# Performance work log

Hardware: AMD Instinct MI355X
Metric: run time of the kernel (lower is better)

Reference implementation:

```python
import jax, jax.numpy as jnp
import numpy as np

H, KVH, HD = 16, 8, 64
EPS = 1e-6
SCALING = HD ** -0.5


def _rms_norm(x, w):
    # RMSNorm over last dim (head_dim)
    var = jnp.mean(x * x, axis=-1, keepdims=True)
    return x * jax.lax.rsqrt(var + EPS) * w


def _rotate_half(x):
    x1, x2 = jnp.split(x, 2, axis=-1)
    return jnp.concatenate([-x2, x1], axis=-1)


def setup_inputs() -> dict:
    key = jax.random.key(0)
    ks = jax.random.split(key, 12)
    B, Q, CTX, HID = 1, 2048, 2048, 1024
    NB, T = 32, 64  # Q == NB * T
    TOTAL = CTX + Q
    inp = {}
    inp["hidden_states"] = jax.random.normal(ks[0], (B, Q, HID), jnp.float32)
    inp["target_hidden"] = jax.random.normal(ks[1], (B, CTX, HID), jnp.float32)
    pos = jnp.arange(TOTAL, dtype=jnp.float32)[:, None]
    inv = 1.0 / (10000.0 ** (jnp.arange(0, HD, 2, dtype=jnp.float32) / HD))
    ang = pos * inv[None, :]
    emb = jnp.concatenate([ang, ang], axis=-1)
    inp["cos"] = jnp.cos(emb)[None]  # [B, TOTAL, HD]
    inp["sin"] = jnp.sin(emb)[None]
    inp["attention_mask"] = jnp.zeros((B, 1, Q, TOTAL), jnp.float32)
    s = 0.02
    inp["Wq"] = jax.random.normal(ks[2], (HID, H * HD), jnp.float32) * s
    inp["Wk"] = jax.random.normal(ks[3], (HID, KVH * HD), jnp.float32) * s
    inp["Wv"] = jax.random.normal(ks[4], (HID, KVH * HD), jnp.float32) * s
    inp["Wo"] = jax.random.normal(ks[5], (H * HD, HID), jnp.float32) * s
    inp["q_norm_w"] = jnp.ones((HD,), jnp.float32)
    inp["k_norm_w"] = jnp.ones((HD,), jnp.float32)
    inp["tree_bias"] = jax.random.normal(ks[6], (64, H), jnp.float32) * s
    inp["relation_map"] = jax.random.randint(ks[7], (B, NB, T, T), 0, 64, jnp.int32)
    return inp


def reference(hidden_states, target_hidden, cos, sin, attention_mask,
              Wq, Wk, Wv, Wo, q_norm_w, k_norm_w, tree_bias, relation_map):
    B, Q, HID = hidden_states.shape
    CTX = target_hidden.shape[1]
    TOTAL = CTX + Q
    NB, T = relation_map.shape[1], relation_map.shape[2]
    groups = H // KVH

    q = (hidden_states @ Wq).reshape(B, Q, H, HD)
    k_ctx = target_hidden @ Wk
    k_noise = hidden_states @ Wk
    v_ctx = target_hidden @ Wv
    v_noise = hidden_states @ Wv
    k = jnp.concatenate([k_ctx, k_noise], axis=1).reshape(B, TOTAL, KVH, HD)
    v = jnp.concatenate([v_ctx, v_noise], axis=1).reshape(B, TOTAL, KVH, HD)

    q = _rms_norm(q, q_norm_w).transpose(0, 2, 1, 3)  # [B,H,Q,HD]
    k = _rms_norm(k, k_norm_w).transpose(0, 2, 1, 3)  # [B,KVH,TOTAL,HD]
    v = v.transpose(0, 2, 1, 3)

    cos_b = cos[:, None]  # [B,1,TOTAL,HD]
    sin_b = sin[:, None]
    q = q * cos_b[..., -Q:, :] + _rotate_half(q) * sin_b[..., -Q:, :]
    k = k * cos_b + _rotate_half(k) * sin_b

    # GQA: repeat kv heads
    k = jnp.repeat(k, groups, axis=1)  # [B,H,TOTAL,HD]
    v = jnp.repeat(v, groups, axis=1)

    scores = jnp.einsum('bhqd,bhkd->bhqk', q, k) * SCALING  # [B,H,Q,TOTAL]
    scores = scores + attention_mask

    # tree positional bias: block-diagonal (same tree) on the noise-noise block
    bias = tree_bias[relation_map]                 # [B,NB,T,T,H]
    bias = jnp.transpose(bias, (0, 4, 1, 2, 3))    # [B,H,NB,T,T]
    s_noise = scores[..., CTX:].reshape(B, H, NB, T, NB, T)
    idx = jnp.arange(NB)
    s_noise = s_noise.at[:, :, idx, :, idx, :].add(jnp.transpose(bias, (2, 0, 1, 3, 4)))
    scores = jnp.concatenate([scores[..., :CTX], s_noise.reshape(B, H, Q, Q)], axis=-1)

    attn = jax.nn.softmax(scores, axis=-1)
    out = jnp.einsum('bhqk,bhkd->bhqd', attn, v)   # [B,H,Q,HD]
    out = out.transpose(0, 2, 1, 3).reshape(B, Q, H * HD)
    return out @ Wo
```

## Files before the change

kernel.cpp:

```cpp
#include <hip/hip_runtime.h>
#include <hip/hip_bf16.h>

typedef __bf16 bf16x8 __attribute__((ext_vector_type(8)));
typedef float  f32x4  __attribute__((ext_vector_type(4)));

__device__ inline unsigned short f2bf(float f) {
    unsigned int u = __float_as_uint(f);
    u += 0x7fffu + ((u >> 16) & 1u);
    return (unsigned short)(u >> 16);
}
__device__ inline float bf2f(unsigned int s) {
    return __uint_as_float(s << 16);
}
__device__ inline unsigned int pk2bf(float a, float b) {
    __hip_bfloat162 h = __float22bfloat162_rn(make_float2(a, b));
    union { __hip_bfloat162 h; unsigned int u; } cv;
    cv.h = h;
    return cv.u;
}
__device__ inline f32x4 mfma16(bf16x8 a, bf16x8 b, f32x4 c) {
    return __builtin_amdgcn_mfma_f32_16x16x32_bf16(a, b, c, 0, 0, 0);
}
__device__ inline void gload_lds16(const void* g, void* l) {
    __builtin_amdgcn_global_load_lds(
        (const __attribute__((address_space(1))) void*)g,
        (__attribute__((address_space(3))) void*)l, 16, 0, 0);
}

__global__ __launch_bounds__(256) void prep1(const float* __restrict__ th, const float* __restrict__ hs,
                                             const float* __restrict__ Wk, const float* __restrict__ Wv,
                                             const float* __restrict__ Wq, const float* __restrict__ Wo,
                                             unsigned short* __restrict__ X,
                                             unsigned short* __restrict__ Wkvt,
                                             unsigned short* __restrict__ Wqt,
                                             unsigned short* __restrict__ Wot) {
    __shared__ float t[64][65];
    int bx = blockIdx.x, tid = threadIdx.x;
    if (bx < 4096) {
        int i = bx * 256 + tid;
        const int n4 = 2048 * 1024 / 4;
        float4 v = (i < n4) ? ((const float4*)th)[i] : ((const float4*)hs)[i - n4];
        ((uint2*)X)[i] = make_uint2(pk2bf(v.x, v.y), pk2bf(v.z, v.w));
        return;
    }
    int t4 = bx - 4096;
    const float* in; unsigned short* out; int in_rs, xt, yt;
    if (t4 < 256)      { in = Wq; out = Wqt; in_rs = 1024; xt = t4 & 15; yt = t4 >> 4; }
    else if (t4 < 512) { t4 -= 256; in = Wo; out = Wot; in_rs = 1024; xt = t4 & 15; yt = t4 >> 4; }
    else if (t4 < 640) { t4 -= 512; in = Wk; out = Wkvt; in_rs = 512; xt = t4 & 7; yt = t4 >> 3; }
    else               { t4 -= 640; in = Wv; out = Wkvt + (size_t)512 * 1024; in_rs = 512; xt = t4 & 7; yt = t4 >> 3; }
    int r0 = yt * 64, c0b = xt * 64;
    int rr = tid >> 4, c4 = (tid & 15) * 4;
#pragma unroll
    for (int i = 0; i < 4; i++) {
        int r = rr + 16 * i;
        float4 v = *(const float4*)&in[(size_t)(r0 + r) * in_rs + c0b + c4];
        t[c4][r] = v.x; t[c4 + 1][r] = v.y; t[c4 + 2][r] = v.z; t[c4 + 3][r] = v.w;
    }
    __syncthreads();
#pragma unroll
    for (int i = 0; i < 4; i++) {
        int cc = rr + 16 * i;
        *(uint2*)&out[(size_t)(c0b + cc) * 1024 + r0 + c4] =
            make_uint2(pk2bf(t[cc][c4], t[cc][c4 + 1]), pk2bf(t[cc][c4 + 2], t[cc][c4 + 3]));
    }
}

union GemmLds {
    struct { unsigned short A[2][128 * 64]; unsigned short B[2][64 * 64]; } s;
    unsigned short Ost[128 * 72];
};

template <bool FP32OUT>
__device__ __forceinline__ void gemm_bk64(const unsigned short* __restrict__ A,
                                          const unsigned short* __restrict__ Bt,
                                          int m0, int n0,
                                          unsigned short* __restrict__ dstBf, int dstStride,
                                          const float* __restrict__ nw,
                                          const float* __restrict__ cosb,
                                          const float* __restrict__ sinb,
                                          int posBase, float scale,
                                          float* __restrict__ dstF,
                                          GemmLds* u) {
    int tid = threadIdx.x, wave = tid >> 6, lane = tid & 63, quad = lane >> 4, l16 = lane & 15;
    f32x4 acc[2][4] = {};

    int drow = lane >> 3;
    int sch = ((lane & 7) ^ drow) * 8;
    const unsigned short* AgB = A + (size_t)(m0 + wave * 32 + drow) * 1024 + sch;
    const unsigned short* BgB = Bt + (size_t)(n0 + wave * 16 + drow) * 1024 + sch;

    auto dma = [&](int k0, int b) {
#pragma unroll
        for (int ii = 0; ii < 4; ii++)
            gload_lds16(AgB + (size_t)ii * 8 * 1024 + k0, &u->s.A[b][(wave * 32 + ii * 8) * 64]);
#pragma unroll
        for (int jj = 0; jj < 2; jj++)
            gload_lds16(BgB + (size_t)jj * 8 * 1024 + k0, &u->s.B[b][(wave * 16 + jj * 8) * 64]);
    };
    dma(0, 0);

    for (int kt = 0; kt < 16; kt++) {
        int b = kt & 1;
        __syncthreads();
        if (kt < 15) dma((kt + 1) * 64, b ^ 1);
#pragma unroll
        for (int kk = 0; kk < 2; kk++) {
            int co = ((kk * 4 + quad) ^ (l16 & 7)) * 8;
            bf16x8 af0 = *(const bf16x8*)&u->s.A[b][(wave * 32 + l16) * 64 + co];
            bf16x8 af1 = *(const bf16x8*)&u->s.A[b][(wave * 32 + 16 + l16) * 64 + co];
            bf16x8 bq[4];
#pragma unroll
            for (int ng = 0; ng < 4; ng++)
                bq[ng] = *(const bf16x8*)&u->s.B[b][(ng * 16 + l16) * 64 + co];
#pragma unroll
            for (int ng = 0; ng < 4; ng++) {
                acc[0][ng] = mfma16(af0, bq[ng], acc[0][ng]);
                acc[1][ng] = mfma16(af1, bq[ng], acc[1][ng]);
            }
        }
    }

    if constexpr (FP32OUT) {
#pragma unroll
        for (int i = 0; i < 2; i++)
#pragma unroll
            for (int j = 0; j < 4; j++) {
                int m = m0 + wave * 32 + i * 16 + quad * 4;
                int n = n0 + j * 16 + l16;
#pragma unroll
                for (int r = 0; r < 4; r++)
                    dstF[(size_t)(m + r) * 1024 + n] = acc[i][j][r];
            }
        return;
    }

    __syncthreads();
    unsigned short* Ost = u->Ost;
    int c0 = l16, c1 = 16 + l16, c2 = 32 + l16, c3 = 48 + l16;
    if (nw) {
        float w0 = nw[c0], w1 = nw[c1], w2 = nw[c2], w3 = nw[c3];
#pragma unroll
        for (int i = 0; i < 2; i++) {
            float s[4];
#pragma unroll
            for (int r = 0; r < 4; r++)
                s[r] = acc[i][0][r] * acc[i][0][r] + acc[i][1][r] * acc[i][1][r] +
                       acc[i][2][r] * acc[i][2][r] + acc[i][3][r] * acc[i][3][r];
#pragma unroll
            for (int m = 1; m <= 8; m <<= 1) {
#pragma unroll
                for (int r = 0; r < 4; r++) s[r] += __shfl_xor(s[r], m);
            }
#pragma unroll
            for (int r = 0; r < 4; r++) {
                float rn = rsqrtf(s[r] * (1.0f / 64.0f) + 1e-6f);
                int row = wave * 32 + i * 16 + quad * 4 + r;
                size_t pos = (size_t)(posBase + m0 + row) * 64;
                float x0 = acc[i][0][r] * rn * w0, x1 = acc[i][1][r] * rn * w1;
                float x2 = acc[i][2][r] * rn * w2, x3 = acc[i][3][r] * rn * w3;
                float y0 = fmaf(x0, cosb[pos + c0], -x2 * sinb[pos + c0]) * scale;
                float y1 = fmaf(x1, cosb[pos + c1], -x3 * sinb[pos + c1]) * scale;
                float y2 = fmaf(x2, cosb[pos + c2],  x0 * sinb[pos + c2]) * scale;
                float y3 = fmaf(x3, cosb[pos + c3],  x1 * sinb[pos + c3]) * scale;
                Ost[row * 72 + c0] = f2bf(y0);
                Ost[row * 72 + c1] = f2bf(y1);
                Ost[row * 72 + c2] = f2bf(y2);
                Ost[row * 72 + c3] = f2bf(y3);
            }
        }
    } else {
#pragma unroll
        for (int i = 0; i < 2; i++)
#pragma unroll
            for (int r = 0; r < 4; r++) {
                int row = wave * 32 + i * 16 + quad * 4 + r;
                Ost[row * 72 + c0] = f2bf(acc[i][0][r]);
                Ost[row * 72 + c1] = f2bf(acc[i][1][r]);
                Ost[row * 72 + c2] = f2bf(acc[i][2][r]);
                Ost[row * 72 + c3] = f2bf(acc[i][3][r]);
            }
    }
    __syncthreads();
    int row = tid >> 3, c = (tid & 7) * 8;
#pragma unroll
    for (int i = 0; i < 4; i++) {
        int rr = row + 32 * i;
        uint4 val = *(uint4*)&Ost[rr * 72 + c];
        *(uint4*)&dstBf[(size_t)(m0 + rr) * dstStride + c] = val;
    }
}

__global__ __launch_bounds__(256) void gemm_qkv(const unsigned short* __restrict__ X,
                                                const unsigned short* __restrict__ Wkvt,
                                                const unsigned short* __restrict__ Wqt,
                                                const float* __restrict__ qnw,
                                                const float* __restrict__ knw,
                                                const float* __restrict__ cosb,
                                                const float* __restrict__ sinb,
                                                unsigned short* __restrict__ Qb,
                                                unsigned short* __restrict__ Kb,
                                                unsigned short* __restrict__ Vraw) {
    __shared__ GemmLds u;
    int bx = blockIdx.x, ny = blockIdx.y;
    if (bx < 32) {
        if (ny < 8)
            gemm_bk64<false>(X, Wkvt, bx * 128, ny * 64,
                             Kb + (size_t)ny * 4096 * 64, 64, knw, cosb, sinb, 0, 1.0f, nullptr, &u);
        else
            gemm_bk64<false>(X, Wkvt, bx * 128, ny * 64,
                             Vraw + (ny - 8) * 64, 512, nullptr, nullptr, nullptr, 0, 1.0f, nullptr, &u);
    } else {
        gemm_bk64<false>(X + (size_t)2048 * 1024, Wqt, (bx - 32) * 128, ny * 64,
                         Qb + (size_t)ny * 2048 * 64, 64, qnw, cosb, sinb, 2048,
                         0.18033688011112042f, nullptr, &u);
    }
}

__global__ __launch_bounds__(256) void gemm_wo(const unsigned short* __restrict__ A,
                                               const unsigned short* __restrict__ Bt,
                                               float* __restrict__ C) {
    __shared__ GemmLds u;
    gemm_bk64<true>(A, Bt, blockIdx.x * 128, blockIdx.y * 64,
                    nullptr, 0, nullptr, nullptr, nullptr, 0, 1.0f, C, &u);
}

__global__ __launch_bounds__(256) void vtrans(const unsigned short* __restrict__ Vraw,
                                              unsigned short* __restrict__ Vtr) {
    __shared__ float t[64][65];
    int t4 = blockIdx.x;
    int xk = t4 & 63, z = t4 >> 6;
    const unsigned short* ip = Vraw + (size_t)xk * 64 * 512 + z * 64;
    unsigned short* op = Vtr + (size_t)z * 64 * 4096 + (size_t)xk * 64;
    int tid = threadIdx.x, rr = tid >> 4, c0 = (tid & 15) * 4;
#pragma unroll
    for (int i = 0; i < 4; i++) {
        int r = rr + 16 * i;
        uint2 v = *(const uint2*)&ip[(size_t)r * 512 + c0];
        t[c0][r]     = bf2f(v.x & 0xffff);
        t[c0 + 1][r] = bf2f(v.x >> 16);
        t[c0 + 2][r] = bf2f(v.y & 0xffff);
        t[c0 + 3][r] = bf2f(v.y >> 16);
    }
    __syncthreads();
#pragma unroll
    for (int i = 0; i < 4; i++) {
        int d = rr + 16 * i;
        *(uint2*)&op[(size_t)d * 4096 + c0] =
            make_uint2(pk2bf(t[d][c0], t[d][c0 + 1]), pk2bf(t[d][c0 + 2], t[d][c0 + 3]));
    }
}

__global__ __launch_bounds__(256) void attn7(const unsigned short* __restrict__ Qb,
                                             const unsigned short* __restrict__ Kb,
                                             const unsigned short* __restrict__ Vt,
                                             const int* __restrict__ relmap,
                                             const float* __restrict__ tree_bias,
                                             unsigned short* __restrict__ Opart,
                                             float* __restrict__ Lpart) {
    __shared__ alignas(16) union {
        struct { unsigned short K[2][4096]; unsigned short V[2][4096]; unsigned short P[4][2048]; } s;
        unsigned short O[128 * 72];
    } u;

    int qt = blockIdx.x, h = blockIdx.y, ks = blockIdx.z, kvh = h >> 1;
    int tid = threadIdx.x, wave = tid >> 6, lane = tid & 63, quad = lane >> 4, l16 = lane & 15;

    bf16x8 qf[2][2];
#pragma unroll
    for (int qg = 0; qg < 2; qg++) {
        int q = qt * 128 + wave * 32 + qg * 16 + l16;
        const unsigned short* qp = Qb + ((size_t)h * 2048 + q) * 64 + quad * 8;
        qf[qg][0] = *(const bf16x8*)qp;
        qf[qg][1] = *(const bf16x8*)(qp + 32);
    }
    f32x4 o[4][2] = {};
    f32x4 lacc[2] = {};
    union { unsigned short us[8]; bf16x8 v; } one_u;
#pragma unroll
    for (int i = 0; i < 8; i++) one_u.us[i] = 0x3F80;
    const bf16x8 ones = one_u.v;

    int drow = lane >> 3;
    int sch = ((lane & 7) ^ drow) * 8;
    const unsigned short* KgB = Kb + ((size_t)kvh * 4096 + ks * 1024) * 64;
    const unsigned short* VgB = Vt + (size_t)kvh * 64 * 4096 + ks * 1024;
    int r0 = wave * 16, r1 = r0 + 8;
    const unsigned short* Kg0 = KgB + (size_t)(r0 + drow) * 64 + sch;
    const unsigned short* Kg1 = KgB + (size_t)(r1 + drow) * 64 + sch;
    const unsigned short* Vg0 = VgB + (size_t)(r0 + drow) * 4096 + sch;
    const unsigned short* Vg1 = VgB + (size_t)(r1 + drow) * 4096 + sch;

    auto dma = [&](int kt, int b) {
        gload_lds16(Kg0 + kt * 4096, &u.s.K[b][r0 * 64]);
        gload_lds16(Kg1 + kt * 4096, &u.s.K[b][r1 * 64]);
        gload_lds16(Vg0 + kt * 64, &u.s.V[b][r0 * 64]);
        gload_lds16(Vg1 + kt * 64, &u.s.V[b][r1 * 64]);
    };
    dma(0, 0);

    unsigned short* pw = &u.s.P[wave][0];
    int sw = l16 & 7;
    int psw = (l16 & 7) * 2;
    int nb = 2 * qt + (wave >> 1);
    int bias_kt = 32 + nb - ks * 16;
    const float LOG2E = 1.4426950408889634f;

    for (int kt = 0; kt < 16; kt++) {
        int b = kt & 1;
        __syncthreads();
        if (kt + 1 < 16) dma(kt + 1, b ^ 1);

#pragma unroll
        for (int g = 0; g < 4; g++) {
            int krow = (g * 16 + l16) * 64;
            bf16x8 kf0 = *(const bf16x8*)&u.s.K[b][krow + ((quad ^ sw) * 8)];
            bf16x8 kf1 = *(const bf16x8*)&u.s.K[b][krow + (((4 + quad) ^ sw) * 8)];
            float pv[2][4];
#pragma unroll
            for (int qg = 0; qg < 2; qg++) {
                f32x4 s = {};
                s = mfma16(kf0, qf[qg][0], s);
                s = mfma16(kf1, qf[qg][1], s);
#pragma unroll
                for (int r = 0; r < 4; r++) pv[qg][r] = s[r];
            }
            if (kt == bias_kt) {
#pragma unroll
                for (int qg = 0; qg < 2; qg++)
#pragma unroll
                    for (int r = 0; r < 4; r++) {
                        int t1 = (wave & 1) * 32 + qg * 16 + l16;
                        int t2 = g * 16 + quad * 4 + r;
                        int rel = relmap[nb * 4096 + t1 * 64 + t2];
                        pv[qg][r] += tree_bias[rel * 16 + h] * LOG2E;
                    }
            }
#pragma unroll
            for (int qg = 0; qg < 2; qg++) {
                float p0 = __builtin_amdgcn_exp2f(pv[qg][0]);
                float p1 = __builtin_amdgcn_exp2f(pv[qg][1]);
                float p2 = __builtin_amdgcn_exp2f(pv[qg][2]);
                float p3 = __builtin_amdgcn_exp2f(pv[qg][3]);
                *(uint2*)&pw[(qg * 16 + l16) * 64 + (((g * 4 + quad) ^ psw) * 4)] =
                    make_uint2(pk2bf(p0, p1), pk2bf(p2, p3));
            }
        }
        bf16x8 pf[2][2];
#pragma unroll
        for (int qg = 0; qg < 2; qg++) {
            pf[qg][0] = *(const bf16x8*)&pw[(qg * 16 + l16) * 64 + (((quad * 2) ^ psw) * 4)];
            pf[qg][1] = *(const bf16x8*)&pw[(qg * 16 + l16) * 64 + (((8 + quad * 2) ^ psw) * 4)];
            lacc[qg] = mfma16(ones, pf[qg][0], lacc[qg]);
            lacc[qg] = mfma16(ones, pf[qg][1], lacc[qg]);
        }
#pragma unroll
        for (int dg = 0; dg < 4; dg++) {
            int vrow = (dg * 16 + l16) * 64;
            bf16x8 vf0 = *(const bf16x8*)&u.s.V[b][vrow + ((quad ^ sw) * 8)];
            bf16x8 vf1 = *(const bf16x8*)&u.s.V[b][vrow + (((4 + quad) ^ sw) * 8)];
#pragma unroll
            for (int qg = 0; qg < 2; qg++) {
                o[dg][qg] = mfma16(vf0, pf[qg][0], o[dg][qg]);
                o[dg][qg] = mfma16(vf1, pf[qg][1], o[dg][qg]);
            }
        }
    }
    __syncthreads();

    float lv0 = lacc[0][0], lv1 = lacc[1][0];
#pragma unroll
    for (int qg = 0; qg < 2; qg++) {
        int qlocal = wave * 32 + qg * 16 + l16;
#pragma unroll
        for (int dg = 0; dg < 4; dg++) {
            f32x4 ov = o[dg][qg];
            *(uint2*)&u.O[qlocal * 72 + dg * 16 + quad * 4] =
                make_uint2(pk2bf(ov[0], ov[1]), pk2bf(ov[2], ov[3]));
        }
        if (quad == 0)
            Lpart[((size_t)ks * 16 + h) * 2048 + qt * 128 + qlocal] = qg ? lv1 : lv0;
    }
    __syncthreads();
    int row = tid >> 3, c = (tid & 7) * 8;
#pragma unroll
    for (int i = 0; i < 4; i++) {
        int rr = row + 32 * i;
        uint4 val = *(uint4*)&u.O[rr * 72 + c];
        size_t q = qt * 128 + rr;
        *(uint4*)&Opart[((size_t)ks * 2048 + q) * 1024 + h * 64 + c] = val;
    }
}

__global__ __launch_bounds__(256) void combine4(const unsigned short* __restrict__ Op,
                                                const float* __restrict__ Lp,
                                                unsigned short* __restrict__ AO) {
    int t = blockIdx.x * 256 + threadIdx.x;
    int q = t >> 7, h = (t >> 3) & 15, c8 = (t & 7) * 8;
    size_t base = ((size_t)q * 16 + h) * 64 + c8;
    float s[8] = {};
    float l = 0.0f;
#pragma unroll
    for (int ks = 0; ks < 4; ks++) {
        uint4 v = *(const uint4*)&Op[(size_t)ks * 2097152 + base];
        s[0] += bf2f(v.x & 0xffff); s[1] += bf2f(v.x >> 16);
        s[2] += bf2f(v.y & 0xffff); s[3] += bf2f(v.y >> 16);
        s[4] += bf2f(v.z & 0xffff); s[5] += bf2f(v.z >> 16);
        s[6] += bf2f(v.w & 0xffff); s[7] += bf2f(v.w >> 16);
        l += Lp[((size_t)ks * 16 + h) * 2048 + q];
    }
    float inv = 1.0f / l;
    uint4 r;
    r.x = pk2bf(s[0] * inv, s[1] * inv);
    r.y = pk2bf(s[2] * inv, s[3] * inv);
    r.z = pk2bf(s[4] * inv, s[5] * inv);
    r.w = pk2bf(s[6] * inv, s[7] * inv);
    *(uint4*)&AO[base] = r;
}

extern "C" void kernel_launch(void* const* d_in, const int* in_sizes, int n_in,
                              void* d_out, int out_size, void* d_ws, size_t ws_size,
                              hipStream_t stream) {
    const float* hs   = (const float*)d_in[0];
    const float* th   = (const float*)d_in[1];
    const float* cosb = (const float*)d_in[2];
    const float* sinb = (const float*)d_in[3];
    const float* Wq  = (const float*)d_in[5];
    const float* Wk  = (const float*)d_in[6];
    const float* Wv  = (const float*)d_in[7];
    const float* Wo  = (const float*)d_in[8];
    const float* qnw = (const float*)d_in[9];
    const float* knw = (const float*)d_in[10];
    const float* tb  = (const float*)d_in[11];
    const int*   rm  = (const int*)d_in[12];
    float* out = (float*)d_out;

    char* ws = (char*)d_ws;
    size_t off = 0;
    auto alloc = [&](size_t b) { char* p = ws + off; off += (b + 255) & ~(size_t)255; return p; };
    char*           pool  = alloc((size_t)16 * 1024 * 1024);
    unsigned short* X     = (unsigned short*)pool;
    unsigned short* Vraw  = (unsigned short*)(pool + (size_t)8 * 1024 * 1024);
    unsigned short* Opart = (unsigned short*)pool;
    unsigned short* Wqt   = (unsigned short*)alloc((size_t)1024 * 1024 * 2);
    unsigned short* Wkvt  = (unsigned short*)alloc((size_t)1024 * 1024 * 2);
    unsigned short* Wot   = (unsigned short*)alloc((size_t)1024 * 1024 * 2);
    unsigned short* Qb    = (unsigned short*)alloc((size_t)16 * 2048 * 64 * 2);
    unsigned short* Kb    = (unsigned short*)alloc((size_t)8 * 4096 * 64 * 2);
    unsigned short* Vtr   = (unsigned short*)alloc((size_t)8 * 64 * 4096 * 2);
    unsigned short* AOb   = (unsigned short*)alloc((size_t)2048 * 1024 * 2);
    float*          Lpart = (float*)alloc((size_t)4 * 16 * 2048 * 4);

    prep1<<<4864, 256, 0, stream>>>(th, hs, Wk, Wv, Wq, Wo, X, Wkvt, Wqt, Wot);
    gemm_qkv<<<dim3(48, 16), 256, 0, stream>>>(X, Wkvt, Wqt, qnw, knw, cosb, sinb, Qb, Kb, Vraw);
    vtrans<<<512, 256, 0, stream>>>(Vraw, Vtr);
    attn7<<<dim3(16, 16, 4), 256, 0, stream>>>(Qb, Kb, Vtr, rm, tb, Opart, Lpart);
    combine4<<<1024, 256, 0, stream>>>(Opart, Lpart, AOb);
    gemm_wo<<<dim3(16, 16), 256, 0, stream>>>(AOb, Wot, out);
}
```

Measured before the change: 204.9 us.

## Fuse V transpose into QKV GEMM, single-buffer V in attention, smaller Wo tiles

```diff
diff --git a/kernel.cpp b/kernel.cpp
--- a/kernel.cpp
+++ b/kernel.cpp
@@ -71,7 +71,6 @@
     unsigned short Ost[128 * 72];
 };
 
-template <bool FP32OUT>
 __device__ __forceinline__ void gemm_bk64(const unsigned short* __restrict__ A,
                                           const unsigned short* __restrict__ Bt,
                                           int m0, int n0,
@@ -80,7 +79,7 @@
                                           const float* __restrict__ cosb,
                                           const float* __restrict__ sinb,
                                           int posBase, float scale,
-                                          float* __restrict__ dstF,
+                                          unsigned short* __restrict__ vtrDst,
                                           GemmLds* u) {
     int tid = threadIdx.x, wave = tid >> 6, lane = tid & 63, quad = lane >> 4, l16 = lane & 15;
     f32x4 acc[2][4] = {};
@@ -119,20 +118,6 @@
                 acc[1][ng] = mfma16(af1, bq[ng], acc[1][ng]);
             }
         }
-    }
-
-    if constexpr (FP32OUT) {
-#pragma unroll
-        for (int i = 0; i < 2; i++)
-#pragma unroll
-            for (int j = 0; j < 4; j++) {
-                int m = m0 + wave * 32 + i * 16 + quad * 4;
-                int n = n0 + j * 16 + l16;
-#pragma unroll
-                for (int r = 0; r < 4; r++)
-                    dstF[(size_t)(m + r) * 1024 + n] = acc[i][j][r];
-            }
-        return;
     }
 
     __syncthreads();
@@ -182,6 +167,21 @@
             }
     }
     __syncthreads();
+    if (vtrDst) {
+        int d = tid >> 2, kseg = tid & 3;
+        unsigned short* vrow = vtrDst + (size_t)d * 4096 + m0 + kseg * 32;
+#pragma unroll
+        for (int c = 0; c < 4; c++) {
+            int kb = kseg * 32 + c * 8;
+            uint4 w;
+            w.x = (unsigned int)Ost[(kb + 0) * 72 + d] | ((unsigned int)Ost[(kb + 1) * 72 + d] << 16);
+            w.y = (unsigned int)Ost[(kb + 2) * 72 + d] | ((unsigned int)Ost[(kb + 3) * 72 + d] << 16);
+            w.z = (unsigned int)Ost[(kb + 4) * 72 + d] | ((unsigned int)Ost[(kb + 5) * 72 + d] << 16);
+            w.w = (unsigned int)Ost[(kb + 6) * 72 + d] | ((unsigned int)Ost[(kb + 7) * 72 + d] << 16);
+            *(uint4*)(vrow + c * 8) = w;
+        }
+        return;
+    }
     int row = tid >> 3, c = (tid & 7) * 8;
 #pragma unroll
     for (int i = 0; i < 4; i++) {
@@ -200,66 +200,78 @@
                                                 const float* __restrict__ sinb,
                                                 unsigned short* __restrict__ Qb,
                                                 unsigned short* __restrict__ Kb,
-                                                unsigned short* __restrict__ Vraw) {
+                                                unsigned short* __restrict__ Vtr) {
     __shared__ GemmLds u;
-    int bx = blockIdx.x, ny = blockIdx.y;
+    int ny = blockIdx.x, bx = blockIdx.y;
     if (bx < 32) {
         if (ny < 8)
-            gemm_bk64<false>(X, Wkvt, bx * 128, ny * 64,
-                             Kb + (size_t)ny * 4096 * 64, 64, knw, cosb, sinb, 0, 1.0f, nullptr, &u);
+            gemm_bk64(X, Wkvt, bx * 128, ny * 64,
+                      Kb + (size_t)ny * 4096 * 64, 64, knw, cosb, sinb, 0, 1.0f, nullptr, &u);
         else
-            gemm_bk64<false>(X, Wkvt, bx * 128, ny * 64,
-                             Vraw + (ny - 8) * 64, 512, nullptr, nullptr, nullptr, 0, 1.0f, nullptr, &u);
+            gemm_bk64(X, Wkvt, bx * 128, ny * 64,
+                      nullptr, 0, nullptr, nullptr, nullptr, 0, 1.0f,
+                      Vtr + (size_t)(ny - 8) * 64 * 4096, &u);
     } else {
-        gemm_bk64<false>(X + (size_t)2048 * 1024, Wqt, (bx - 32) * 128, ny * 64,
-                         Qb + (size_t)ny * 2048 * 64, 64, qnw, cosb, sinb, 2048,
-                         0.18033688011112042f, nullptr, &u);
-    }
-}
-
-__global__ __launch_bounds__(256) void gemm_wo(const unsigned short* __restrict__ A,
-                                               const unsigned short* __restrict__ Bt,
-                                               float* __restrict__ C) {
-    __shared__ GemmLds u;
-    gemm_bk64<true>(A, Bt, blockIdx.x * 128, blockIdx.y * 64,
-                    nullptr, 0, nullptr, nullptr, nullptr, 0, 1.0f, C, &u);
-}
-
-__global__ __launch_bounds__(256) void vtrans(const unsigned short* __restrict__ Vraw,
-                                              unsigned short* __restrict__ Vtr) {
-    __shared__ float t[64][65];
-    int t4 = blockIdx.x;
-    int xk = t4 & 63, z = t4 >> 6;
-    const unsigned short* ip = Vraw + (size_t)xk * 64 * 512 + z * 64;
-    unsigned short* op = Vtr + (size_t)z * 64 * 4096 + (size_t)xk * 64;
-    int tid = threadIdx.x, rr = tid >> 4, c0 = (tid & 15) * 4;
-#pragma unroll
-    for (int i = 0; i < 4; i++) {
-        int r = rr + 16 * i;
-        uint2 v = *(const uint2*)&ip[(size_t)r * 512 + c0];
-        t[c0][r]     = bf2f(v.x & 0xffff);
-        t[c0 + 1][r] = bf2f(v.x >> 16);
-        t[c0 + 2][r] = bf2f(v.y & 0xffff);
-        t[c0 + 3][r] = bf2f(v.y >> 16);
-    }
-    __syncthreads();
-#pragma unroll
-    for (int i = 0; i < 4; i++) {
-        int d = rr + 16 * i;
-        *(uint2*)&op[(size_t)d * 4096 + c0] =
-            make_uint2(pk2bf(t[d][c0], t[d][c0 + 1]), pk2bf(t[d][c0 + 2], t[d][c0 + 3]));
-    }
-}
-
-__global__ __launch_bounds__(256) void attn7(const unsigned short* __restrict__ Qb,
-                                             const unsigned short* __restrict__ Kb,
-                                             const unsigned short* __restrict__ Vt,
-                                             const int* __restrict__ relmap,
-                                             const float* __restrict__ tree_bias,
-                                             unsigned short* __restrict__ Opart,
-                                             float* __restrict__ Lpart) {
+        gemm_bk64(X + (size_t)2048 * 1024, Wqt, (bx - 32) * 128, ny * 64,
+                  Qb + (size_t)ny * 2048 * 64, 64, qnw, cosb, sinb, 2048,
+                  0.18033688011112042f, nullptr, &u);
+    }
+}
+
+__global__ __launch_bounds__(256) void gemm_wo64(const unsigned short* __restrict__ A,
+                                                 const unsigned short* __restrict__ Bt,
+                                                 float* __restrict__ C) {
+    __shared__ struct { unsigned short A[2][4096]; unsigned short B[2][4096]; } u;
+    int m0 = blockIdx.x * 64, n0 = blockIdx.y * 64;
+    int tid = threadIdx.x, wave = tid >> 6, lane = tid & 63, quad = lane >> 4, l16 = lane & 15;
+    f32x4 acc[4] = {};
+
+    int drow = lane >> 3;
+    int sch = ((lane & 7) ^ drow) * 8;
+    const unsigned short* Ag0 = A + (size_t)(m0 + wave * 16 + drow) * 1024 + sch;
+    const unsigned short* Bg0 = Bt + (size_t)(n0 + wave * 16 + drow) * 1024 + sch;
+
+    auto dma = [&](int k0, int b) {
+        gload_lds16(Ag0 + k0, &u.A[b][(wave * 16) * 64]);
+        gload_lds16(Ag0 + (size_t)8 * 1024 + k0, &u.A[b][(wave * 16 + 8) * 64]);
+        gload_lds16(Bg0 + k0, &u.B[b][(wave * 16) * 64]);
+        gload_lds16(Bg0 + (size_t)8 * 1024 + k0, &u.B[b][(wave * 16 + 8) * 64]);
+    };
+    dma(0, 0);
+
+    for (int kt = 0; kt < 16; kt++) {
+        int b = kt & 1;
+        __syncthreads();
+        if (kt < 15) dma((kt + 1) * 64, b ^ 1);
+#pragma unroll
+        for (int kk = 0; kk < 2; kk++) {
+            int co = ((kk * 4 + quad) ^ (l16 & 7)) * 8;
+            bf16x8 af = *(const bf16x8*)&u.A[b][(wave * 16 + l16) * 64 + co];
+#pragma unroll
+            for (int ng = 0; ng < 4; ng++) {
+                bf16x8 bq = *(const bf16x8*)&u.B[b][(ng * 16 + l16) * 64 + co];
+                acc[ng] = mfma16(af, bq, acc[ng]);
+            }
+        }
+    }
+#pragma unroll
+    for (int j = 0; j < 4; j++) {
+        int n = n0 + j * 16 + l16;
+#pragma unroll
+        for (int r = 0; r < 4; r++)
+            C[(size_t)(m0 + wave * 16 + quad * 4 + r) * 1024 + n] = acc[j][r];
+    }
+}
+
+__global__ __launch_bounds__(256, 4) void attn5(const unsigned short* __restrict__ Qb,
+                                                const unsigned short* __restrict__ Kb,
+                                                const unsigned short* __restrict__ Vt,
+                                                const int* __restrict__ relmap,
+                                                const float* __restrict__ tree_bias,
+                                                unsigned short* __restrict__ Opart,
+                                                float* __restrict__ Lpart) {
     __shared__ alignas(16) union {
-        struct { unsigned short K[2][4096]; unsigned short V[2][4096]; unsigned short P[4][2048]; } s;
+        struct { unsigned short K[2][4096]; unsigned short V[4096]; unsigned short P[4][2048]; } s;
         unsigned short O[128 * 72];
     } u;
 
@@ -291,13 +303,8 @@
     const unsigned short* Vg0 = VgB + (size_t)(r0 + drow) * 4096 + sch;
     const unsigned short* Vg1 = VgB + (size_t)(r1 + drow) * 4096 + sch;
 
-    auto dma = [&](int kt, int b) {
-        gload_lds16(Kg0 + kt * 4096, &u.s.K[b][r0 * 64]);
-        gload_lds16(Kg1 + kt * 4096, &u.s.K[b][r1 * 64]);
-        gload_lds16(Vg0 + kt * 64, &u.s.V[b][r0 * 64]);
-        gload_lds16(Vg1 + kt * 64, &u.s.V[b][r1 * 64]);
-    };
-    dma(0, 0);
+    gload_lds16(Kg0, &u.s.K[0][r0 * 64]);
+    gload_lds16(Kg1, &u.s.K[0][r1 * 64]);
 
     unsigned short* pw = &u.s.P[wave][0];
     int sw = l16 & 7;
@@ -309,7 +316,12 @@
     for (int kt = 0; kt < 16; kt++) {
         int b = kt & 1;
         __syncthreads();
-        if (kt + 1 < 16) dma(kt + 1, b ^ 1);
+        if (kt + 1 < 16) {
+            gload_lds16(Kg0 + (kt + 1) * 4096, &u.s.K[b ^ 1][r0 * 64]);
+            gload_lds16(Kg1 + (kt + 1) * 4096, &u.s.K[b ^ 1][r1 * 64]);
+        }
+        gload_lds16(Vg0 + kt * 64, &u.s.V[r0 * 64]);
+        gload_lds16(Vg1 + kt * 64, &u.s.V[r1 * 64]);
 
 #pragma unroll
         for (int g = 0; g < 4; g++) {
@@ -346,6 +358,8 @@
                     make_uint2(pk2bf(p0, p1), pk2bf(p2, p3));
             }
         }
+        __syncthreads();
+
         bf16x8 pf[2][2];
 #pragma unroll
         for (int qg = 0; qg < 2; qg++) {
@@ -357,8 +371,8 @@
 #pragma unroll
         for (int dg = 0; dg < 4; dg++) {
             int vrow = (dg * 16 + l16) * 64;
-            bf16x8 vf0 = *(const bf16x8*)&u.s.V[b][vrow + ((quad ^ sw) * 8)];
-            bf16x8 vf1 = *(const bf16x8*)&u.s.V[b][vrow + (((4 + quad) ^ sw) * 8)];
+            bf16x8 vf0 = *(const bf16x8*)&u.s.V[vrow + ((quad ^ sw) * 8)];
+            bf16x8 vf1 = *(const bf16x8*)&u.s.V[vrow + (((4 + quad) ^ sw) * 8)];
 #pragma unroll
             for (int qg = 0; qg < 2; qg++) {
                 o[dg][qg] = mfma16(vf0, pf[qg][0], o[dg][qg]);
@@ -440,7 +454,6 @@
     auto alloc = [&](size_t b) { char* p = ws + off; off += (b + 255) & ~(size_t)255; return p; };
     char*           pool  = alloc((size_t)16 * 1024 * 1024);
     unsigned short* X     = (unsigned short*)pool;
-    unsigned short* Vraw  = (unsigned short*)(pool + (size_t)8 * 1024 * 1024);
     unsigned short* Opart = (unsigned short*)pool;
     unsigned short* Wqt   = (unsigned short*)alloc((size_t)1024 * 1024 * 2);
     unsigned short* Wkvt  = (unsigned short*)alloc((size_t)1024 * 1024 * 2);
@@ -452,9 +465,8 @@
     float*          Lpart = (float*)alloc((size_t)4 * 16 * 2048 * 4);
 
     prep1<<<4864, 256, 0, stream>>>(th, hs, Wk, Wv, Wq, Wo, X, Wkvt, Wqt, Wot);
-    gemm_qkv<<<dim3(48, 16), 256, 0, stream>>>(X, Wkvt, Wqt, qnw, knw, cosb, sinb, Qb, Kb, Vraw);
-    vtrans<<<512, 256, 0, stream>>>(Vraw, Vtr);
-    attn7<<<dim3(16, 16, 4), 256, 0, stream>>>(Qb, Kb, Vtr, rm, tb, Opart, Lpart);
+    gemm_qkv<<<dim3(16, 48), 256, 0, stream>>>(X, Wkvt, Wqt, qnw, knw, cosb, sinb, Qb, Kb, Vtr);
+    attn5<<<dim3(16, 16, 4), 256, 0, stream>>>(Qb, Kb, Vtr, rm, tb, Opart, Lpart);
     combine4<<<1024, 256, 0, stream>>>(Opart, Lpart, AOb);
-    gemm_wo<<<dim3(16, 16), 256, 0, stream>>>(AOb, Wot, out);
-}
+    gemm_wo64<<<dim3(32, 16), 256, 0, stream>>>(AOb, Wot, out);
+}
```

Measured after the change: 191.5 us. 6.5% less time.
